# Optimization experiments

Hardware: AMD Instinct MI355X
Metric: run time of the kernel (lower is better)

## Reference

```python
import jax, jax.numpy as jnp
import numpy as np

C = 768
HEADS = 12

def setup_inputs() -> dict:
    key = jax.random.key(0)
    k1, k2, k3 = jax.random.split(key, 3)
    x = jax.random.normal(k1, (8, C, 32, 32), dtype=jnp.float32)
    # 1x1 convs are channel-wise linear maps; store as [out_c, in_c]
    w_qkv = jax.random.normal(k2, (3 * C, C), dtype=jnp.float32) * (C ** -0.5)
    w_proj = jax.random.normal(k3, (C, C), dtype=jnp.float32) * (C ** -0.5)
    return {"x": x, "w_qkv": w_qkv, "w_proj": w_proj}

def reference(x, w_qkv, w_proj):
    b, c, h, w = x.shape
    heads = HEADS
    dh = c // heads
    n = h * w
    scale = dh ** -0.5
    # 1x1 conv QKV: [b, 3c, h, w] -> [b, 3, heads, dh, n]
    qkv = jnp.einsum('oc,bchw->bohw', w_qkv, x).reshape(b, 3, heads, dh, n)
    q, k, v = qkv[:, 0], qkv[:, 1], qkv[:, 2]  # each [b, heads, dh, n]
    attn = jnp.einsum('bhdn,bhdm->bhnm', q, k) * scale  # [b, heads, n, n]
    attn = jax.nn.softmax(attn, axis=-1)
    out = jnp.einsum('bhnm,bhdm->bhdn', attn, v)  # [b, heads, dh, n]
    out = out.reshape(b, c, h, w)
    return jnp.einsum('oc,bchw->bohw', w_proj, out)
```

## Files before the change

### kernel.cpp

```cpp
#include <hip/hip_runtime.h>

typedef unsigned short u16;
typedef unsigned int u32;
typedef float v4f __attribute__((ext_vector_type(4)));
typedef __bf16 bf16x8 __attribute__((ext_vector_type(8)));

#define BATCH 8
#define CDIM 768
#define NHEAD 12
#define DH 64
#define NSEQ 1024
#define SCL 0.18033688011112042f

__device__ __forceinline__ u16 f2bf(float f) {
  u32 u = __builtin_bit_cast(u32, f);
  u += 0x7fffu + ((u >> 16) & 1u);
  return (u16)(u >> 16);
}

__device__ __forceinline__ u16 b16(float f) {
  return (u16)((__builtin_bit_cast(u32, f) + 0x8000u) >> 16);
}
__device__ __forceinline__ u32 pkbf(float hi, float lo) {
  u32 a = __builtin_bit_cast(u32, hi) + 0x8000u;
  u32 b = __builtin_bit_cast(u32, lo) + 0x8000u;
  return __builtin_amdgcn_perm(a, b, 0x07060302u);
}

__device__ __forceinline__ v4f mfma16(bf16x8 a, bf16x8 b, v4f c) {
  return __builtin_amdgcn_mfma_f32_16x16x32_bf16(a, b, c, 0, 0, 0);
}

__device__ __forceinline__ void gload16(const u16* g, u16* l) {
  __builtin_amdgcn_global_load_lds(
      (const __attribute__((address_space(1))) void*)g,
      (__attribute__((address_space(3))) void*)l, 16, 0, 0);
}

__global__ __launch_bounds__(256) void k_prep(const float* __restrict__ x,
                                              const float* __restrict__ wq,
                                              const float* __restrict__ wp,
                                              u16* __restrict__ xT,
                                              u16* __restrict__ wqb,
                                              u16* __restrict__ wpb) {
  __shared__ u16 Ts[64][72];
  int bid = blockIdx.x;
  int t = threadIdx.x;
  if (bid < 2304) {
    bool isQ = bid < 1728;
    const float* s = isQ ? wq : wp;
    u16* d = isQ ? wqb : wpb;
    int i = (isQ ? bid : bid - 1728) * 256 + t;
    float4 v = ((const float4*)s)[i];
    u32 lo = (u32)f2bf(v.x) | ((u32)f2bf(v.y) << 16);
    u32 hi = (u32)f2bf(v.z) | ((u32)f2bf(v.w) << 16);
    ((uint2*)d)[i] = uint2{lo, hi};
    return;
  }
  int id = bid - 2304;
  int p0 = (id & 15) * 64; id >>= 4;
  int c0 = (id % 12) * 64; int b = id / 12;
  int cr = t >> 4;
  int p4 = (t & 15) * 4;
  const float* src = x + ((size_t)b * CDIM + c0) * NSEQ + p0;
#pragma unroll
  for (int i = 0; i < 4; ++i) {
    int c = cr + i * 16;
    float4 v = *(const float4*)&src[(size_t)c * NSEQ + p4];
    Ts[p4 + 0][c] = f2bf(v.x);
    Ts[p4 + 1][c] = f2bf(v.y);
    Ts[p4 + 2][c] = f2bf(v.z);
    Ts[p4 + 3][c] = f2bf(v.w);
  }
  __syncthreads();
  int p = t >> 2;
  int cq = t & 3;
  u16* dst = xT + ((size_t)b * NSEQ + p0 + p) * CDIM + c0;
#pragma unroll
  for (int j = 0; j < 2; ++j) {
    int ch = cq + j * 4;
    *(int4*)&dst[ch * 8] = *(const int4*)&Ts[p][ch * 8];
  }
}

__global__ __launch_bounds__(256) void k_gemm_qkv(const u16* __restrict__ Wb,
                                                  const u16* __restrict__ xT,
                                                  u16* __restrict__ qkT,
                                                  u16* __restrict__ vbuf) {
  int oT = blockIdx.x * 128, pT = blockIdx.y * 128, b = blockIdx.z;
  __shared__ u16 As[2][128 * 32];
  __shared__ u16 Bs[2][128 * 32];
  int t = threadIdx.x, lane = t & 63, wid = t >> 6;
  int ln = lane & 15, quad = lane >> 4;
  int wr = wid >> 1, wc = wid & 1;
  v4f acc[4][4] = {};

  int lr = lane >> 2, lc = (lane & 3) * 8;
  const u16* Ag = Wb + (size_t)(oT + wid * 16 + lr) * CDIM + lc;
  const u16* Bg = xT + ((size_t)b * NSEQ + pT + wid * 16 + lr) * CDIM + lc;
  int s0 = (wid * 16) * 32, s1 = (wid * 16 + 64) * 32;

  gload16(Ag, &As[0][s0]);
  gload16(Ag + (size_t)64 * CDIM, &As[0][s1]);
  gload16(Bg, &Bs[0][s0]);
  gload16(Bg + (size_t)64 * CDIM, &Bs[0][s1]);
  __syncthreads();

  for (int k = 0; k < 24; ++k) {
    int cur = k & 1, nxt = cur ^ 1;
    if (k < 23) {
      int kk = (k + 1) * 32;
      gload16(Ag + kk, &As[nxt][s0]);
      gload16(Ag + (size_t)64 * CDIM + kk, &As[nxt][s1]);
      gload16(Bg + kk, &Bs[nxt][s0]);
      gload16(Bg + (size_t)64 * CDIM + kk, &Bs[nxt][s1]);
    }
    bf16x8 af[4], bfr[4];
#pragma unroll
    for (int mt = 0; mt < 4; ++mt)
      af[mt] = *(const bf16x8*)&As[cur][(wr * 64 + mt * 16 + ln) * 32 + quad * 8];
#pragma unroll
    for (int nt = 0; nt < 4; ++nt)
      bfr[nt] = *(const bf16x8*)&Bs[cur][(wc * 64 + nt * 16 + ln) * 32 + quad * 8];
#pragma unroll
    for (int mt = 0; mt < 4; ++mt)
#pragma unroll
      for (int nt = 0; nt < 4; ++nt)
        acc[mt][nt] = mfma16(af[mt], bfr[nt], acc[mt][nt]);
    __syncthreads();
  }

  bool isV = (oT >= 2 * CDIM);
#pragma unroll
  for (int mt = 0; mt < 4; ++mt) {
#pragma unroll
    for (int nt = 0; nt < 4; ++nt) {
      int ro = oT + wr * 64 + mt * 16 + quad * 4;
      int cp = pT + wc * 64 + nt * 16 + ln;
      if (!isV) {
        u32 lo = (u32)f2bf(acc[mt][nt][0]) | ((u32)f2bf(acc[mt][nt][1]) << 16);
        u32 hi = (u32)f2bf(acc[mt][nt][2]) | ((u32)f2bf(acc[mt][nt][3]) << 16);
        *(uint2*)&qkT[((size_t)b * NSEQ + cp) * 1536 + ro] = uint2{lo, hi};
      } else {
#pragma unroll
        for (int r = 0; r < 4; ++r)
          vbuf[((size_t)b * CDIM + (ro - 2 * CDIM + r)) * NSEQ + cp] =
              f2bf(acc[mt][nt][r]);
      }
    }
  }
}

__global__ __launch_bounds__(256) void k_attn(const u16* __restrict__ qkT,
                                              const u16* __restrict__ vbuf,
                                              u16* __restrict__ attnT) {
  int id = blockIdx.x;
  int b = id & 7;
  int j = id >> 3;
  int h = j % 12;
  int nt0 = (j / 12) * 128;

  int t = threadIdx.x, lane = t & 63, wid = t >> 6;
  int ln = lane & 15, quad = lane >> 4;
  int nbase = nt0 + wid * 32;

  __shared__ u16 Ks[2][64 * 32];
  __shared__ u16 Vs[2][64 * 32];
  __shared__ u16 Pa[4][32 * 72];
  u16* myP = Pa[wid];

  const u16* qbase = qkT + ((size_t)b * NSEQ + nbase) * 1536 + h * DH;
  bf16x8 aq[2][2];
#pragma unroll
  for (int mt = 0; mt < 2; ++mt)
#pragma unroll
    for (int ks = 0; ks < 2; ++ks)
      aq[mt][ks] = *(const bf16x8*)&qbase[(size_t)(mt * 16 + ln) * 1536 + ks * 32 + quad * 8];

  bf16x8 ones;
#pragma unroll
  for (int i = 0; i < 8; ++i) ones[i] = __builtin_bit_cast(__bf16, (u16)0x3F80);

  v4f oacc[2][4] = {};
  v4f lacc[2] = {};

  int lr = lane >> 2, lc = (lane & 3) * 8;
  const u16* kgw = qkT + (size_t)b * NSEQ * 1536 + CDIM + h * DH +
                   (size_t)(wid * 16 + lr) * 1536 + lc;
  const u16* vgw = vbuf + ((size_t)b * CDIM + h * DH + wid * 16 + lr) * NSEQ + lc;
  int sb = (wid * 16) * 32;

  for (int s = 0; s < 16; ++s) {
    __syncthreads();
    size_t ko = (size_t)s * 64 * 1536;
    int vo = s * 64;
    gload16(kgw + ko, &Ks[0][sb]);
    gload16(kgw + ko + 32, &Ks[1][sb]);
    gload16(vgw + vo, &Vs[0][sb]);
    gload16(vgw + vo + 32, &Vs[1][sb]);
    __syncthreads();

#pragma unroll
    for (int ct = 0; ct < 4; ++ct) {
      bf16x8 kf0 = *(const bf16x8*)&Ks[0][(ct * 16 + ln) * 32 + quad * 8];
      bf16x8 kf1 = *(const bf16x8*)&Ks[1][(ct * 16 + ln) * 32 + quad * 8];
#pragma unroll
      for (int mt = 0; mt < 2; ++mt) {
        v4f sc = {};
        sc = mfma16(kf0, aq[mt][0], sc);
        sc = mfma16(kf1, aq[mt][1], sc);
        float p0 = __builtin_amdgcn_exp2f(sc[0] * SCL);
        float p1 = __builtin_amdgcn_exp2f(sc[1] * SCL);
        float p2 = __builtin_amdgcn_exp2f(sc[2] * SCL);
        float p3 = __builtin_amdgcn_exp2f(sc[3] * SCL);
        *(uint2*)&myP[(mt * 16 + ln) * 72 + ct * 16 + quad * 4] =
            uint2{pkbf(p1, p0), pkbf(p3, p2)};
      }
    }

    bf16x8 ap[2][2];
#pragma unroll
    for (int mt = 0; mt < 2; ++mt)
#pragma unroll
      for (int ks = 0; ks < 2; ++ks)
        ap[mt][ks] = *(const bf16x8*)&myP[(mt * 16 + ln) * 72 + ks * 32 + quad * 8];
#pragma unroll
    for (int mt = 0; mt < 2; ++mt) {
      lacc[mt] = mfma16(ap[mt][0], ones, lacc[mt]);
      lacc[mt] = mfma16(ap[mt][1], ones, lacc[mt]);
    }
#pragma unroll
    for (int nt = 0; nt < 4; ++nt) {
      bf16x8 vf0 = *(const bf16x8*)&Vs[0][(nt * 16 + ln) * 32 + quad * 8];
      bf16x8 vf1 = *(const bf16x8*)&Vs[1][(nt * 16 + ln) * 32 + quad * 8];
#pragma unroll
      for (int mt = 0; mt < 2; ++mt) {
        oacc[mt][nt] = mfma16(ap[mt][0], vf0, oacc[mt][nt]);
        oacc[mt][nt] = mfma16(ap[mt][1], vf1, oacc[mt][nt]);
      }
    }
  }

#pragma unroll
  for (int mt = 0; mt < 2; ++mt) {
#pragma unroll
    for (int r = 0; r < 4; ++r) {
      float inv = 1.0f / lacc[mt][r];
      int n = nbase + mt * 16 + quad * 4 + r;
      u16* dst = attnT + ((size_t)b * NSEQ + n) * CDIM + h * DH;
#pragma unroll
      for (int nt = 0; nt < 4; ++nt)
        dst[nt * 16 + ln] = b16(oacc[mt][nt][r] * inv);
    }
  }
}

__global__ __launch_bounds__(256) void k_gemm_proj(const u16* __restrict__ Wb,
                                                   const u16* __restrict__ aT,
                                                   float* __restrict__ out) {
  int b = blockIdx.x, oT = blockIdx.y * 128, pT = blockIdx.z * 128;
  __shared__ u16 As[2][128 * 32];
  __shared__ u16 Bs[2][128 * 32];
  int t = threadIdx.x, lane = t & 63, wid = t >> 6;
  int ln = lane & 15, quad = lane >> 4;
  int wr = wid >> 1, wc = wid & 1;
  v4f acc[4][4] = {};

  int lr = lane >> 2, lc = (lane & 3) * 8;
  const u16* Ag = Wb + (size_t)(oT + wid * 16 + lr) * CDIM + lc;
  const u16* Bg = aT + ((size_t)b * NSEQ + pT + wid * 16 + lr) * CDIM + lc;
  int a0 = (wid * 16) * 32, a1 = (wid * 16 + 64) * 32;

  gload16(Ag, &As[0][a0]);
  gload16(Ag + (size_t)64 * CDIM, &As[0][a1]);
  gload16(Bg, &Bs[0][a0]);
  gload16(Bg + (size_t)64 * CDIM, &Bs[0][a1]);
  __syncthreads();

  for (int k = 0; k < 24; ++k) {
    int cur = k & 1, nxt = cur ^ 1;
    if (k < 23) {
      int kk = (k + 1) * 32;
      gload16(Ag + kk, &As[nxt][a0]);
      gload16(Ag + (size_t)64 * CDIM + kk, &As[nxt][a1]);
      gload16(Bg + kk, &Bs[nxt][a0]);
      gload16(Bg + (size_t)64 * CDIM + kk, &Bs[nxt][a1]);
    }
    bf16x8 af[4], bfr[4];
#pragma unroll
    for (int mt = 0; mt < 4; ++mt)
      af[mt] = *(const bf16x8*)&As[cur][(wr * 64 + mt * 16 + ln) * 32 + quad * 8];
#pragma unroll
    for (int nt = 0; nt < 4; ++nt)
      bfr[nt] = *(const bf16x8*)&Bs[cur][(wc * 64 + nt * 16 + ln) * 32 + quad * 8];
#pragma unroll
    for (int mt = 0; mt < 4; ++mt)
#pragma unroll
      for (int nt = 0; nt < 4; ++nt)
        acc[mt][nt] = mfma16(af[mt], bfr[nt], acc[mt][nt]);
    __syncthreads();
  }

#pragma unroll
  for (int mt = 0; mt < 4; ++mt) {
#pragma unroll
    for (int nt = 0; nt < 4; ++nt) {
      int ro = oT + wr * 64 + mt * 16 + quad * 4;
      int cp = pT + wc * 64 + nt * 16 + ln;
#pragma unroll
      for (int r = 0; r < 4; ++r)
        out[((size_t)b * CDIM + ro + r) * NSEQ + cp] = acc[mt][nt][r];
    }
  }
}

extern "C" void kernel_launch(void* const* d_in, const int* in_sizes, int n_in,
                              void* d_out, int out_size, void* d_ws, size_t ws_size,
                              hipStream_t stream) {
  const float* x = (const float*)d_in[0];
  const float* w_qkv = (const float*)d_in[1];
  const float* w_proj = (const float*)d_in[2];
  float* out = (float*)d_out;

  char* ws = (char*)d_ws;
  u16* wqkv_bf = (u16*)(ws);
  u16* wproj_bf = (u16*)(ws + 3538944);
  u16* xT = (u16*)(ws + 4718592);
  u16* vbuf = (u16*)(ws + 17301504);
  u16* qkT = (u16*)d_out;
  u16* attnT = xT;

  k_prep<<<dim3(3840), dim3(256), 0, stream>>>(x, w_qkv, w_proj, xT, wqkv_bf, wproj_bf);
  k_gemm_qkv<<<dim3(18, 8, 8), dim3(256), 0, stream>>>(wqkv_bf, xT, qkT, vbuf);
  k_attn<<<dim3(768), dim3(256), 0, stream>>>(qkT, vbuf, attnT);
  k_gemm_proj<<<dim3(8, 6, 8), dim3(256), 0, stream>>>(wproj_bf, attnT, out);
}
```

Before: 196.5 us.

## Replace double-buffered QKV GEMM loop with single-stage 64-wide K step

The QKV projection GEMM no longer prefetches the next K tile during compute. Each iteration now loads a 64-wide K slice into both LDS buffers, synchronizes, and runs twice as many MFMAs. This halves the number of loop iterations and barriers, but load latency is no longer overlapped with compute inside a block, so the kernel depends on other resident blocks to hide memory latency. It also uses more registers for the extra fragments.

```diff
diff --git a/kernel.cpp b/kernel.cpp
--- a/kernel.cpp
+++ b/kernel.cpp
@@ -100,34 +100,36 @@
   const u16* Bg = xT + ((size_t)b * NSEQ + pT + wid * 16 + lr) * CDIM + lc;
   int s0 = (wid * 16) * 32, s1 = (wid * 16 + 64) * 32;
 
-  gload16(Ag, &As[0][s0]);
-  gload16(Ag + (size_t)64 * CDIM, &As[0][s1]);
-  gload16(Bg, &Bs[0][s0]);
-  gload16(Bg + (size_t)64 * CDIM, &Bs[0][s1]);
-  __syncthreads();
-
-  for (int k = 0; k < 24; ++k) {
-    int cur = k & 1, nxt = cur ^ 1;
-    if (k < 23) {
-      int kk = (k + 1) * 32;
-      gload16(Ag + kk, &As[nxt][s0]);
-      gload16(Ag + (size_t)64 * CDIM + kk, &As[nxt][s1]);
-      gload16(Bg + kk, &Bs[nxt][s0]);
-      gload16(Bg + (size_t)64 * CDIM + kk, &Bs[nxt][s1]);
-    }
-    bf16x8 af[4], bfr[4];
+  for (int kk = 0; kk < CDIM; kk += 64) {
+    __syncthreads();
+    gload16(Ag + kk, &As[0][s0]);
+    gload16(Ag + (size_t)64 * CDIM + kk, &As[0][s1]);
+    gload16(Ag + kk + 32, &As[1][s0]);
+    gload16(Ag + (size_t)64 * CDIM + kk + 32, &As[1][s1]);
+    gload16(Bg + kk, &Bs[0][s0]);
+    gload16(Bg + (size_t)64 * CDIM + kk, &Bs[0][s1]);
+    gload16(Bg + kk + 32, &Bs[1][s0]);
+    gload16(Bg + (size_t)64 * CDIM + kk + 32, &Bs[1][s1]);
+    __syncthreads();
+
+    bf16x8 af0[4], af1[4], bf0[4], bf1[4];
+#pragma unroll
+    for (int mt = 0; mt < 4; ++mt) {
+      af0[mt] = *(const bf16x8*)&As[0][(wr * 64 + mt * 16 + ln) * 32 + quad * 8];
+      af1[mt] = *(const bf16x8*)&As[1][(wr * 64 + mt * 16 + ln) * 32 + quad * 8];
+    }
+#pragma unroll
+    for (int nt = 0; nt < 4; ++nt) {
+      bf0[nt] = *(const bf16x8*)&Bs[0][(wc * 64 + nt * 16 + ln) * 32 + quad * 8];
+      bf1[nt] = *(const bf16x8*)&Bs[1][(wc * 64 + nt * 16 + ln) * 32 + quad * 8];
+    }
 #pragma unroll
     for (int mt = 0; mt < 4; ++mt)
-      af[mt] = *(const bf16x8*)&As[cur][(wr * 64 + mt * 16 + ln) * 32 + quad * 8];
-#pragma unroll
-    for (int nt = 0; nt < 4; ++nt)
-      bfr[nt] = *(const bf16x8*)&Bs[cur][(wc * 64 + nt * 16 + ln) * 32 + quad * 8];
-#pragma unroll
-    for (int mt = 0; mt < 4; ++mt)
-#pragma unroll
-      for (int nt = 0; nt < 4; ++nt)
-        acc[mt][nt] = mfma16(af[mt], bfr[nt], acc[mt][nt]);
-    __syncthreads();
+#pragma unroll
+      for (int nt = 0; nt < 4; ++nt) {
+        acc[mt][nt] = mfma16(af0[mt], bf0[nt], acc[mt][nt]);
+        acc[mt][nt] = mfma16(af1[mt], bf1[nt], acc[mt][nt]);
+      }
   }
 
   bool isV = (oT >= 2 * CDIM);
```

Measured after the change: 199.1 us. About the same (+1.3%).
